# Performance work log

Measured on AMD Instinct MI355X. Metric: run time of the kernel, lower is better.

The kernel has to match this reference:

```python
import jax, jax.numpy as jnp
import numpy as np

S = 128    # spatial grid size
B = 2      # batch size
N = 60000  # number of points
EPS = 1e-4 # SparseConvNet BatchNorm eps
NEG = -3.0e38


def _conv3d(x, w, stride, padding):
    return jax.lax.conv_general_dilated(
        x, w, (stride,) * 3, padding,
        dimension_numbers=('NCDHW', 'OIDHW', 'NCDHW'))


def _pool2(x):
    # 2x2x2 max-pool, stride 2 (dims are powers of two)
    b, c, d, h, w = x.shape
    return x.reshape(b, c, d // 2, 2, h // 2, 2, w // 2, 2).max(axis=(3, 5, 7))


def _bn_relu(x, mask, gamma, beta):
    # BatchNormLeakyReLU(leakiness=0) over ACTIVE sites only (SCN semantics)
    n = mask.sum()
    mu = (x * mask).sum(axis=(0, 2, 3, 4)) / n
    mu_ = mu[None, :, None, None, None]
    var = (((x - mu_) ** 2) * mask).sum(axis=(0, 2, 3, 4)) / n
    scale = (gamma / jnp.sqrt(var + EPS))[None, :, None, None, None]
    y = (x - mu_) * scale + beta[None, :, None, None, None]
    return jnp.maximum(y, 0.0) * mask


def setup_inputs() -> dict:
    key = jax.random.key(0)
    ks = jax.random.split(key, 10)
    bi = jax.random.randint(ks[0], (N,), 0, B)
    xyz = jax.random.randint(ks[1], (N, 3), 0, S)
    feat = jax.random.normal(ks[2], (N, 1), dtype=jnp.float32)
    point_cloud = jnp.concatenate(
        [bi[:, None].astype(jnp.float32), xyz.astype(jnp.float32), feat], axis=1)

    def cw(k, o, i, ksz):
        return jax.random.normal(k, (o, i, ksz, ksz, ksz), dtype=jnp.float32) * np.float32(np.sqrt(2.0 / (i * ksz ** 3)))

    w_sub = cw(ks[3], 8, 1, 3)            # SubmanifoldConvolution(1->8, k=3)
    w0 = cw(ks[4], 16, 8, 2)              # Convolution(8->16, k=2, s=2)
    w1 = cw(ks[5], 32, 16, 2)
    w2 = cw(ks[6], 64, 32, 2)
    w3 = cw(ks[7], 128, 64, 2)
    g0, b0 = jnp.ones(8), jnp.zeros(8)
    g1, b1 = jnp.ones(16), jnp.zeros(16)
    g2, b2 = jnp.ones(32), jnp.zeros(32)
    g3, b3 = jnp.ones(64), jnp.zeros(64)
    Wc = jax.random.normal(ks[8], (2, 1024), dtype=jnp.float32) * np.float32(np.sqrt(1.0 / 1024))
    bc = jnp.zeros(2, dtype=jnp.float32)
    return dict(point_cloud=point_cloud, w_sub=w_sub, w0=w0, w1=w1, w2=w2, w3=w3,
                g0=g0, g1=g1, g2=g2, g3=g3, b0=b0, b1=b1, b2=b2, b3=b3, Wc=Wc, bc=bc)


def reference(point_cloud, w_sub, w0, w1, w2, w3,
              g0, g1, g2, g3, b0, b1, b2, b3, Wc, bc):
    bi = point_cloud[:, 0].astype(jnp.int32)
    ix = point_cloud[:, 1].astype(jnp.int32)
    iy = point_cloud[:, 2].astype(jnp.int32)
    iz = point_cloud[:, 3].astype(jnp.int32)
    f = point_cloud[:, 4]

    # InputLayer mode=3: scatter-sum duplicate coordinates into a dense grid
    grid = jnp.zeros((B, 1, S, S, S), jnp.float32).at[bi, 0, ix, iy, iz].add(f)
    mask = jnp.zeros((B, 1, S, S, S), jnp.float32).at[bi, 0, ix, iy, iz].set(1.0)

    # Submanifold conv k=3: dense conv (inactive feats are 0), output only at active sites
    h = _conv3d(grid, w_sub, 1, 'SAME') * mask

    for w, g, b in ((w0, g0, b0), (w1, g1, b1), (w2, g2, b2), (w3, g3, b3)):
        h = _bn_relu(h, mask, g, b)
        h = _conv3d(h, w, 2, 'VALID')
        mask = _pool2(mask)          # output site active iff any input in window active
        h = h * mask

    for _ in range(2):
        h = jnp.where(mask > 0, h, NEG)
        h = _pool2(h)
        mask = _pool2(mask)
        h = jnp.where(mask > 0, h, 0.0)

    # SparseToDense + flatten: [B,128,2,2,2] -> [B,1024]
    x = h.reshape(B, 128 * 8)
    rec_pos = jnp.maximum(x, 0.0) @ Wc.T + bc
    coords = point_cloud[:, 0:4]
    return coords, rec_pos
```

## Files before the change

### kernel.cpp

```cpp
#include <hip/hip_runtime.h>
#include <math.h>


#define NPTS 60000
#define NB 2
#define NEGF -3.0e38f
#define EPSF 1.0e-4f
#define MARKV 0xFFFEu
#define EMPTYV 0xFFFFu

constexpr int NV0 = NB * 128 * 128 * 128;
constexpr int NV1 = NB * 64 * 64 * 64;
constexpr int NV2 = NB * 32 * 32 * 32;
constexpr int NV3 = NB * 16 * 16 * 16;
constexpr int NV4 = NB * 8 * 8 * 8;

constexpr size_t OFF_CNT   = 0;
constexpr size_t OFF_BNSUM = 64;
constexpr size_t OFF_BNSS  = 1088;
constexpr size_t OFF_MASK5 = 2112;
constexpr size_t OFF_FGRID = 4096;
constexpr size_t OFF_IDX0  = OFF_FGRID + (size_t)NV0 * 4;
constexpr size_t OFF_IDX1  = OFF_IDX0 + (size_t)NV0 * 2;
constexpr size_t OFF_IDX2  = OFF_IDX1 + (size_t)NV1 * 2;
constexpr size_t OFF_IDX3  = OFF_IDX2 + (size_t)NV2 * 2;
constexpr size_t OFF_IDX4  = OFF_IDX3 + (size_t)NV3 * 2;
constexpr size_t OFF_LIST0 = OFF_IDX4 + (size_t)NV4 * 2;
constexpr size_t OFF_LIST1 = OFF_LIST0 + (size_t)NPTS * 4;
constexpr size_t OFF_LIST2 = OFF_LIST1 + (size_t)NPTS * 4;
constexpr size_t OFF_LIST3 = OFF_LIST2 + (size_t)NPTS * 4;
constexpr size_t OFF_LIST4 = OFF_LIST3 + (size_t)NV3 * 4;
constexpr size_t OFF_H0 = OFF_LIST4 + (size_t)NV4 * 4;
constexpr size_t OFF_H1 = OFF_H0 + (size_t)NPTS * 8 * 4;
constexpr size_t OFF_H2 = OFF_H1 + (size_t)NPTS * 16 * 4;
constexpr size_t OFF_H3 = OFF_H2 + (size_t)NPTS * 32 * 4;
constexpr size_t OFF_H4 = OFF_H3 + (size_t)NV3 * 64 * 4;
constexpr size_t OFF_H5 = OFF_H4 + (size_t)NV4 * 128 * 4;
constexpr size_t WS_END = OFF_H5 + (size_t)NB * 128 * 64 * 4;


__global__ __launch_bounds__(256) void k_scatter(const float* __restrict__ pc,
                                                 float* __restrict__ fgrid,
                                                 unsigned short* __restrict__ idx0,
                                                 unsigned short* __restrict__ idx1,
                                                 int* __restrict__ wsw,
                                                 float* __restrict__ out) {
  int gid = blockIdx.x * 256 + threadIdx.x;
  if (gid < 528) wsw[gid] = 0;
  idx1[gid] = (unsigned short)EMPTYV;
  if (gid < NPTS) {
    const float* p = pc + (size_t)gid * 5;
    float fb = p[0], fx = p[1], fy = p[2], fz = p[3], f = p[4];
    ((float4*)out)[gid] = make_float4(fb, fx, fy, fz);
    int b = (int)fb, x = (int)fx, y = (int)fy, z = (int)fz;
    int v = ((b * 128 + x) * 128 + y) * 128 + z;
    atomicAdd(&fgrid[v], f);
    idx0[v] = (unsigned short)MARKV;
  }
}

template <int SL, int NCLR16, int NCLRF>
__global__ __launch_bounds__(256) void k_cscan(unsigned short* __restrict__ idx,
                                               int* __restrict__ list,
                                               int* __restrict__ cnt, int slot,
                                               unsigned short* __restrict__ idx_par,
                                               unsigned short* __restrict__ clr16,
                                               float* __restrict__ clrf) {
  constexpr int NV = NB * SL * SL * SL;
  constexpr int NT = NV / 4;
  int gid = blockIdx.x * 256 + threadIdx.x;
  if (NCLR16 > 0 && gid < NCLR16) clr16[gid] = (unsigned short)EMPTYV;
  if (NCLRF > 0) {
    float4 z4 = make_float4(0.f, 0.f, 0.f, 0.f);
    for (int i = gid; i < NCLRF / 4; i += NT) ((float4*)clrf)[i] = z4;
  }
  ushort4 u = ((const ushort4*)idx)[gid];
  int p0 = (u.x == MARKV), p1 = (u.y == MARKV), p2 = (u.z == MARKV), p3 = (u.w == MARKV);
  int c = p0 + p1 + p2 + p3;
  int lane = threadIdx.x & 63, wid = threadIdx.x >> 6;
  int x = c;
#pragma unroll
  for (int off = 1; off < 64; off <<= 1) {
    int y = __shfl_up(x, off, 64);
    if (lane >= off) x += y;
  }
  __shared__ int sw[4];
  __shared__ int sbase;
  if (lane == 63) sw[wid] = x;
  __syncthreads();
  if (threadIdx.x == 0) {
    int r = 0;
#pragma unroll
    for (int w = 0; w < 4; w++) { int t = sw[w]; sw[w] = r; r += t; }
    sbase = r ? atomicAdd(&cnt[slot], r) : 0;
  }
  __syncthreads();
  if (!c) return;
  int my = sbase + sw[wid] + (x - c);
  int v0 = gid * 4;
  int pr[4] = {p0, p1, p2, p3};
#pragma unroll
  for (int j = 0; j < 4; j++) {
    if (pr[j]) {
      int v = v0 + j;
      idx[v] = (unsigned short)my;
      list[my] = v;
      my++;
      int z = v & (SL - 1), y = (v / SL) & (SL - 1),
          xx = (v / (SL * SL)) & (SL - 1), b = v / (SL * SL * SL);
      constexpr int SP = SL / 2;
      int pv = ((b * SP + (xx >> 1)) * SP + (y >> 1)) * SP + (z >> 1);
      idx_par[pv] = (unsigned short)MARKV;
    }
  }
}

__global__ __launch_bounds__(256) void k_ctail(unsigned short* __restrict__ idx3,
                                               unsigned short* __restrict__ idx4,
                                               int* __restrict__ list3,
                                               int* __restrict__ list4,
                                               int* __restrict__ cnt) {
  __shared__ int lc3, lc4;
  int tid = threadIdx.x, lane = tid & 63;
  if (tid == 0) { lc3 = 0; lc4 = 0; }
  __syncthreads();
  for (int v = tid; v < NV3; v += 256) {
    bool p = (idx3[v] == MARKV);
    unsigned long long m = __ballot(p);
    int wb = 0;
    if (lane == 0 && m) wb = atomicAdd(&lc3, __popcll(m));
    wb = __shfl(wb, 0, 64);
    if (p) {
      int id = wb + __popcll(m & ((1ull << lane) - 1));
      idx3[v] = (unsigned short)id;
      list3[id] = v;
      int z = v & 15, y = (v >> 4) & 15, x = (v >> 8) & 15, b = v >> 12;
      int pv = ((b * 8 + (x >> 1)) * 8 + (y >> 1)) * 8 + (z >> 1);
      idx4[pv] = (unsigned short)MARKV;
    }
  }
  __syncthreads();
  for (int v = tid; v < NV4; v += 256) {
    bool p = (idx4[v] == MARKV);
    unsigned long long m = __ballot(p);
    int wb = 0;
    if (lane == 0 && m) wb = atomicAdd(&lc4, __popcll(m));
    wb = __shfl(wb, 0, 64);
    if (p) {
      int id = wb + __popcll(m & ((1ull << lane) - 1));
      idx4[v] = (unsigned short)id;
      list4[id] = v;
    }
  }
  __syncthreads();
  if (tid == 0) { cnt[3] = lc3; cnt[4] = lc4; }
}

__global__ __launch_bounds__(256) void k_subconv(const float* __restrict__ fgrid,
                                                 const int* __restrict__ list0,
                                                 const int* __restrict__ cnt,
                                                 const float* __restrict__ wsub,
                                                 float* __restrict__ h0,
                                                 float* __restrict__ bnsum,
                                                 float* __restrict__ bnss) {
  int n = cnt[0];
  if ((int)(blockIdx.x * 256) >= n) return;
  __shared__ float wl[216];
  __shared__ float sbn[16];
  int tid = threadIdx.x;
  for (int i = tid; i < 216; i += 256) wl[i] = wsub[i];
  if (tid < 16) sbn[tid] = 0.f;
  __syncthreads();
  int id = blockIdx.x * 256 + tid;
  bool act = id < n;
  float acc[8] = {0, 0, 0, 0, 0, 0, 0, 0};
  if (act) {
    int v = list0[id];
    int z = v & 127, y = (v >> 7) & 127, x = (v >> 14) & 127, b = v >> 21;
    for (int kd = 0; kd < 3; kd++) {
      int xx = x + kd - 1;
      if ((unsigned)xx >= 128u) continue;
      for (int kh = 0; kh < 3; kh++) {
        int yy = y + kh - 1;
        if ((unsigned)yy >= 128u) continue;
        for (int kw = 0; kw < 3; kw++) {
          int zz = z + kw - 1;
          if ((unsigned)zz >= 128u) continue;
          float val = fgrid[((b * 128 + xx) * 128 + yy) * 128 + zz];
          if (val != 0.f) {
            int t = (kd * 3 + kh) * 3 + kw;
#pragma unroll
            for (int o = 0; o < 8; o++) acc[o] = fmaf(val, wl[o * 27 + t], acc[o]);
          }
        }
      }
    }
#pragma unroll
    for (int o = 0; o < 8; o++) h0[(size_t)id * 8 + o] = acc[o];
  }
  int lane = tid & 63;
#pragma unroll
  for (int o = 0; o < 8; o++) {
    float a = acc[o], q = a * a;
#pragma unroll
    for (int off = 32; off > 0; off >>= 1) {
      a += __shfl_down(a, off, 64);
      q += __shfl_down(q, off, 64);
    }
    if (lane == 0) { atomicAdd(&sbn[o], a); atomicAdd(&sbn[8 + o], q); }
  }
  __syncthreads();
  if (tid < 8) { atomicAdd(&bnsum[tid], sbn[tid]); atomicAdd(&bnss[tid], sbn[8 + tid]); }
}

template <int Ci, int Co, int OCCHUNK, int SLpar, int DENSE_OUT>
__global__ __launch_bounds__(256) void k_conv(const float* __restrict__ hin,
                                              const unsigned short* __restrict__ idxc,
                                              const int* __restrict__ listpar,
                                              const int* __restrict__ cnt,
                                              int slot_bn, int slot_par,
                                              const float* __restrict__ w,
                                              const float* __restrict__ bnsum_in,
                                              const float* __restrict__ bnss_in,
                                              const float* __restrict__ g,
                                              const float* __restrict__ beta,
                                              float* __restrict__ bnsum_out,
                                              float* __restrict__ bnss_out,
                                              float* __restrict__ hout) {
  constexpr int TPP = OCCHUNK / 8;
  constexpr int PPB = 256 / TPP;
  int n = cnt[slot_par];
  if ((int)(blockIdx.x * PPB) >= n) return;
  __shared__ float wl[Ci * 8 * OCCHUNK];
  __shared__ float sl[Ci], bl[Ci];
  __shared__ float bnl[2 * OCCHUNK];
  int tid = threadIdx.x;
  int ocbase = blockIdx.y * OCCHUNK;
  for (int i = tid; i < Ci * 8 * OCCHUNK; i += 256) {
    int ol = i % OCCHUNK;
    int it = i / OCCHUNK;
    int ci = it >> 3, t = it & 7;
    wl[i] = w[((size_t)(ocbase + ol) * Ci + ci) * 8 + t];
  }
  if (tid < Ci) {
    float nn = (float)cnt[slot_bn];
    float mu = bnsum_in[tid] / nn;
    float var = bnss_in[tid] / nn - mu * mu;
    var = fmaxf(var, 0.f);
    float sc = g[tid] / sqrtf(var + EPSF);
    sl[tid] = sc;
    bl[tid] = beta[tid] - mu * sc;
  }
  if (!DENSE_OUT && tid < 2 * OCCHUNK) bnl[tid] = 0.f;
  __syncthreads();
  int pid = blockIdx.x * PPB + tid / TPP;
  int og = tid % TPP;
  bool act = pid < n;
  float acc[8] = {0, 0, 0, 0, 0, 0, 0, 0};
  int Xc = 0, Yc = 0, Zc = 0, bb = 0;
  if (act) {
    int pv = listpar[pid];
    constexpr int SL = SLpar, SC = SLpar * 2;
    Zc = pv & (SL - 1);
    Yc = (pv / SL) & (SL - 1);
    Xc = (pv / (SL * SL)) & (SL - 1);
    bb = pv / (SL * SL * SL);
    for (int t = 0; t < 8; t++) {
      int kd = t >> 2, kh = (t >> 1) & 1, kw = t & 1;
      int cv = ((bb * SC + 2 * Xc + kd) * SC + 2 * Yc + kh) * SC + 2 * Zc + kw;
      unsigned e = idxc[cv];
      if (e >= 0xFFFEu) continue;
      const float* hp = hin + (size_t)e * Ci;
#pragma unroll
      for (int i = 0; i < Ci; i += 4) {
        float4 xv = *(const float4*)(hp + i);
        float y0 = fmaxf(fmaf(xv.x, sl[i + 0], bl[i + 0]), 0.f);
        float y1 = fmaxf(fmaf(xv.y, sl[i + 1], bl[i + 1]), 0.f);
        float y2 = fmaxf(fmaf(xv.z, sl[i + 2], bl[i + 2]), 0.f);
        float y3 = fmaxf(fmaf(xv.w, sl[i + 3], bl[i + 3]), 0.f);
        const float* wp0 = &wl[((i + 0) * 8 + t) * OCCHUNK + og * 8];
        const float* wp1 = &wl[((i + 1) * 8 + t) * OCCHUNK + og * 8];
        const float* wp2 = &wl[((i + 2) * 8 + t) * OCCHUNK + og * 8];
        const float* wp3 = &wl[((i + 3) * 8 + t) * OCCHUNK + og * 8];
#pragma unroll
        for (int o = 0; o < 8; o++) {
          acc[o] = fmaf(y0, wp0[o], acc[o]);
          acc[o] = fmaf(y1, wp1[o], acc[o]);
          acc[o] = fmaf(y2, wp2[o], acc[o]);
          acc[o] = fmaf(y3, wp3[o], acc[o]);
        }
      }
    }
    if (!DENSE_OUT) {
      float* op = hout + (size_t)pid * Co + ocbase + og * 8;
#pragma unroll
      for (int o = 0; o < 8; o++) op[o] = acc[o];
    } else {
      int sp = (Xc * 8 + Yc) * 8 + Zc;
#pragma unroll
      for (int o = 0; o < 8; o++)
        hout[((size_t)bb * 128 + ocbase + og * 8 + o) * 512 + sp] = acc[o];
    }
  }
  if (!DENSE_OUT) {
    int lane = tid & 63;
#pragma unroll
    for (int o = 0; o < 8; o++) {
      float a = acc[o], q = a * a;
#pragma unroll
      for (int off = TPP; off < 64; off <<= 1) {
        a += __shfl_down(a, off, 64);
        q += __shfl_down(q, off, 64);
      }
      if (lane < TPP) {
        atomicAdd(&bnl[lane * 8 + o], a);
        atomicAdd(&bnl[OCCHUNK + lane * 8 + o], q);
      }
    }
    __syncthreads();
    if (tid < OCCHUNK) {
      atomicAdd(&bnsum_out[ocbase + tid], bnl[tid]);
      atomicAdd(&bnss_out[ocbase + tid], bnl[OCCHUNK + tid]);
    }
  }
}

__global__ __launch_bounds__(256) void k_pool1(const float* __restrict__ h4,
                                               const unsigned short* __restrict__ idx4,
                                               float* __restrict__ h5,
                                               int* __restrict__ mask5) {
  int tid = blockIdx.x * 256 + threadIdx.x;
  int sp = tid & 63;
  int c = (tid >> 6) & 127;
  int b = tid >> 13;
  int Z = sp & 3, Y = (sp >> 2) & 3, X = sp >> 4;
  float m = NEGF;
  int any = 0;
#pragma unroll
  for (int t = 0; t < 8; t++) {
    int kd = t >> 2, kh = (t >> 1) & 1, kw = t & 1;
    int csp = ((2 * X + kd) * 8 + 2 * Y + kh) * 8 + 2 * Z + kw;
    if (idx4[b * 512 + csp] != EMPTYV) {
      any = 1;
      m = fmaxf(m, h4[((size_t)b * 128 + c) * 512 + csp]);
    }
  }
  h5[((size_t)b * 128 + c) * 64 + sp] = any ? m : 0.f;
  if (c == 0) mask5[b * 64 + sp] = any;
}

__global__ __launch_bounds__(256) void k_tail(const float* __restrict__ h5,
                                              const int* __restrict__ mask5,
                                              const float* __restrict__ Wc,
                                              const float* __restrict__ bcv,
                                              float* __restrict__ out) {
  __shared__ float h6s[2048];
  int tid = threadIdx.x;
#pragma unroll
  for (int j = 0; j < 8; j++) {
    int e = tid * 8 + j;
    int sp = e & 7, c = (e >> 3) & 127, b = e >> 10;
    int Z = sp & 1, Y = (sp >> 1) & 1, X = sp >> 2;
    float m = NEGF;
    int any = 0;
#pragma unroll
    for (int t = 0; t < 8; t++) {
      int kd = t >> 2, kh = (t >> 1) & 1, kw = t & 1;
      int csp = ((2 * X + kd) * 4 + 2 * Y + kh) * 4 + 2 * Z + kw;
      if (mask5[b * 64 + csp]) {
        any = 1;
        m = fmaxf(m, h5[((size_t)b * 128 + c) * 64 + csp]);
      }
    }
    h6s[e] = any ? fmaxf(m, 0.f) : 0.f;
  }
  __syncthreads();
  int wave = tid >> 6, lane = tid & 63;
  int b = wave >> 1, o = wave & 1;
  float s = 0.f;
  for (int k = lane; k < 1024; k += 64) s += h6s[b * 1024 + k] * Wc[o * 1024 + k];
#pragma unroll
  for (int off = 32; off > 0; off >>= 1) s += __shfl_down(s, off, 64);
  if (lane == 0) out[240000 + b * 2 + o] = s + bcv[o];
}


extern "C" void kernel_launch(void* const* d_in, const int* in_sizes, int n_in,
                              void* d_out, int out_size, void* d_ws, size_t ws_size,
                              hipStream_t stream) {
  const float* pc   = (const float*)d_in[0];
  const float* wsub = (const float*)d_in[1];
  const float* w0   = (const float*)d_in[2];
  const float* w1   = (const float*)d_in[3];
  const float* w2   = (const float*)d_in[4];
  const float* w3   = (const float*)d_in[5];
  const float* g0   = (const float*)d_in[6];
  const float* g1   = (const float*)d_in[7];
  const float* g2   = (const float*)d_in[8];
  const float* g3   = (const float*)d_in[9];
  const float* b0   = (const float*)d_in[10];
  const float* b1   = (const float*)d_in[11];
  const float* b2   = (const float*)d_in[12];
  const float* b3   = (const float*)d_in[13];
  const float* Wc   = (const float*)d_in[14];
  const float* bc   = (const float*)d_in[15];
  float* out = (float*)d_out;

  char* base = (char*)d_ws;
  int*   cnt   = (int*)(base + OFF_CNT);
  float* bnsum = (float*)(base + OFF_BNSUM);
  float* bnss  = (float*)(base + OFF_BNSS);
  int*   mask5 = (int*)(base + OFF_MASK5);
  float* fgrid = (float*)(base + OFF_FGRID);
  unsigned short* idx0 = (unsigned short*)(base + OFF_IDX0);
  unsigned short* idx1 = (unsigned short*)(base + OFF_IDX1);
  unsigned short* idx2 = (unsigned short*)(base + OFF_IDX2);
  unsigned short* idx3 = (unsigned short*)(base + OFF_IDX3);
  unsigned short* idx4 = (unsigned short*)(base + OFF_IDX4);
  int* list0 = (int*)(base + OFF_LIST0);
  int* list1 = (int*)(base + OFF_LIST1);
  int* list2 = (int*)(base + OFF_LIST2);
  int* list3 = (int*)(base + OFF_LIST3);
  int* list4 = (int*)(base + OFF_LIST4);
  float* h0 = (float*)(base + OFF_H0);
  float* h1 = (float*)(base + OFF_H1);
  float* h2 = (float*)(base + OFF_H2);
  float* h3 = (float*)(base + OFF_H3);
  float* h4 = (float*)(base + OFF_H4);
  float* h5 = (float*)(base + OFF_H5);

  hipMemsetAsync(fgrid, 0, (size_t)NV0 * 4, stream);
  hipMemsetAsync(idx0, 0xFF, (size_t)NV0 * 2, stream);

  k_scatter<<<NV1 / 256, 256, 0, stream>>>(pc, fgrid, idx0, idx1, (int*)base, out);

  k_cscan<128, NV2, 0><<<NV0 / 4 / 256, 256, 0, stream>>>(
      idx0, list0, cnt, 0, idx1, idx2, (float*)nullptr);
  k_cscan<64, NV3 + NV4, 0><<<NV1 / 4 / 256, 256, 0, stream>>>(
      idx1, list1, cnt, 1, idx2, idx3, (float*)nullptr);
  k_cscan<32, 0, NV4 * 128><<<NV2 / 4 / 256, 256, 0, stream>>>(
      idx2, list2, cnt, 2, idx3, (unsigned short*)nullptr, h4);
  k_ctail<<<1, 256, 0, stream>>>(idx3, idx4, list3, list4, cnt);

  k_subconv<<<(NPTS + 255) / 256, 256, 0, stream>>>(fgrid, list0, cnt, wsub, h0,
                                                    bnsum + 0, bnss + 0);

  k_conv<8, 16, 16, 64, 0><<<dim3((NPTS + 127) / 128, 1), 256, 0, stream>>>(
      h0, idx0, list1, cnt, 0, 1, w0, bnsum + 0, bnss + 0, g0, b0,
      bnsum + 64, bnss + 64, h1);
  k_conv<16, 32, 32, 32, 0><<<dim3((NPTS + 63) / 64, 1), 256, 0, stream>>>(
      h1, idx1, list2, cnt, 1, 2, w1, bnsum + 64, bnss + 64, g1, b1,
      bnsum + 128, bnss + 128, h2);
  k_conv<32, 64, 32, 16, 0><<<dim3((NV3 + 63) / 64, 2), 256, 0, stream>>>(
      h2, idx2, list3, cnt, 2, 3, w2, bnsum + 128, bnss + 128, g2, b2,
      bnsum + 192, bnss + 192, h3);
  k_conv<64, 128, 16, 8, 1><<<dim3((NV4 + 127) / 128, 8), 256, 0, stream>>>(
      h3, idx3, list4, cnt, 3, 4, w3, bnsum + 192, bnss + 192, g3, b3,
      (float*)nullptr, (float*)nullptr, h4);

  k_pool1<<<(NB * 128 * 64) / 256, 256, 0, stream>>>(h4, idx4, h5, mask5);
  k_tail<<<1, 256, 0, stream>>>(h5, mask5, Wc, bc, out);
}
```

Before: 317.6 us.

## Shard BN atomics across slots, persistent scan blocks, split subconv taps

Batch-norm statistics are now accumulated into 16 slot-strided copies chosen by block index, and the consumer sums the slots. This cuts same-address atomic contention. The compaction scans now run with far fewer blocks, each thread handling several ushort4 chunks, which reduces the number of global counter atomics. The submanifold conv splits the 27 taps across 4 threads per point and combines the partial sums with xor shuffles. Clears are vectorized, and the workspace layout is enlarged to hold the slots. The costs are more scan work per thread and an extra reduction pass in each conv prologue.

```diff
diff --git a/kernel.cpp b/kernel.cpp
--- a/kernel.cpp
+++ b/kernel.cpp
@@ -8,6 +8,7 @@
 #define EPSF 1.0e-4f
 #define MARKV 0xFFFEu
 #define EMPTYV 0xFFFFu
+#define NSLOT 16
 
 constexpr int NV0 = NB * 128 * 128 * 128;
 constexpr int NV1 = NB * 64 * 64 * 64;
@@ -16,10 +17,10 @@
 constexpr int NV4 = NB * 8 * 8 * 8;
 
 constexpr size_t OFF_CNT   = 0;
-constexpr size_t OFF_BNSUM = 64;
-constexpr size_t OFF_BNSS  = 1088;
-constexpr size_t OFF_MASK5 = 2112;
-constexpr size_t OFF_FGRID = 4096;
+constexpr size_t OFF_BNSUM = 1024;
+constexpr size_t OFF_BNSS  = 17408;
+constexpr size_t OFF_MASK5 = 33792;
+constexpr size_t OFF_FGRID = 65536;
 constexpr size_t OFF_IDX0  = OFF_FGRID + (size_t)NV0 * 4;
 constexpr size_t OFF_IDX1  = OFF_IDX0 + (size_t)NV0 * 2;
 constexpr size_t OFF_IDX2  = OFF_IDX1 + (size_t)NV1 * 2;
@@ -46,8 +47,14 @@
                                                  int* __restrict__ wsw,
                                                  float* __restrict__ out) {
   int gid = blockIdx.x * 256 + threadIdx.x;
-  if (gid < 528) wsw[gid] = 0;
-  idx1[gid] = (unsigned short)EMPTYV;
+  if (gid < 2112) {
+    ((int4*)wsw)[gid] = make_int4(0, 0, 0, 0);
+  }
+  if (gid < NV1 / 4) {
+    ((ushort4*)idx1)[gid] =
+        make_ushort4((unsigned short)EMPTYV, (unsigned short)EMPTYV,
+                     (unsigned short)EMPTYV, (unsigned short)EMPTYV);
+  }
   if (gid < NPTS) {
     const float* p = pc + (size_t)gid * 5;
     float fb = p[0], fx = p[1], fy = p[2], fz = p[3], f = p[4];
@@ -59,7 +66,7 @@
   }
 }
 
-template <int SL, int NCLR16, int NCLRF>
+template <int SL, int NBLK, int NCLR16, int NCLRF>
 __global__ __launch_bounds__(256) void k_cscan(unsigned short* __restrict__ idx,
                                                int* __restrict__ list,
                                                int* __restrict__ cnt, int slot,
@@ -67,17 +74,29 @@
                                                unsigned short* __restrict__ clr16,
                                                float* __restrict__ clrf) {
   constexpr int NV = NB * SL * SL * SL;
-  constexpr int NT = NV / 4;
-  int gid = blockIdx.x * 256 + threadIdx.x;
-  if (NCLR16 > 0 && gid < NCLR16) clr16[gid] = (unsigned short)EMPTYV;
+  constexpr int NT = NBLK * 256;
+  constexpr int IT = NV / 4 / NT;
+  int tid = threadIdx.x;
+  int gid = blockIdx.x * 256 + tid;
+  if (NCLR16 > 0) {
+    ushort4 e4 = make_ushort4((unsigned short)EMPTYV, (unsigned short)EMPTYV,
+                              (unsigned short)EMPTYV, (unsigned short)EMPTYV);
+    for (int i = gid; i < NCLR16 / 4; i += NT) ((ushort4*)clr16)[i] = e4;
+  }
   if (NCLRF > 0) {
     float4 z4 = make_float4(0.f, 0.f, 0.f, 0.f);
     for (int i = gid; i < NCLRF / 4; i += NT) ((float4*)clrf)[i] = z4;
   }
-  ushort4 u = ((const ushort4*)idx)[gid];
-  int p0 = (u.x == MARKV), p1 = (u.y == MARKV), p2 = (u.z == MARKV), p3 = (u.w == MARKV);
-  int c = p0 + p1 + p2 + p3;
-  int lane = threadIdx.x & 63, wid = threadIdx.x >> 6;
+  const ushort4* idx4p = (const ushort4*)idx;
+  ushort4 uu[IT];
+  int c = 0;
+#pragma unroll
+  for (int it = 0; it < IT; it++) {
+    uu[it] = idx4p[gid + it * NT];
+    c += (uu[it].x == MARKV) + (uu[it].y == MARKV) + (uu[it].z == MARKV) +
+         (uu[it].w == MARKV);
+  }
+  int lane = tid & 63, wid = tid >> 6;
   int x = c;
 #pragma unroll
   for (int off = 1; off < 64; off <<= 1) {
@@ -88,7 +107,7 @@
   __shared__ int sbase;
   if (lane == 63) sw[wid] = x;
   __syncthreads();
-  if (threadIdx.x == 0) {
+  if (tid == 0) {
     int r = 0;
 #pragma unroll
     for (int w = 0; w < 4; w++) { int t = sw[w]; sw[w] = r; r += t; }
@@ -97,20 +116,23 @@
   __syncthreads();
   if (!c) return;
   int my = sbase + sw[wid] + (x - c);
-  int v0 = gid * 4;
-  int pr[4] = {p0, p1, p2, p3};
-#pragma unroll
-  for (int j = 0; j < 4; j++) {
-    if (pr[j]) {
-      int v = v0 + j;
-      idx[v] = (unsigned short)my;
-      list[my] = v;
-      my++;
-      int z = v & (SL - 1), y = (v / SL) & (SL - 1),
-          xx = (v / (SL * SL)) & (SL - 1), b = v / (SL * SL * SL);
-      constexpr int SP = SL / 2;
-      int pv = ((b * SP + (xx >> 1)) * SP + (y >> 1)) * SP + (z >> 1);
-      idx_par[pv] = (unsigned short)MARKV;
+#pragma unroll
+  for (int it = 0; it < IT; it++) {
+    unsigned short us[4] = {uu[it].x, uu[it].y, uu[it].z, uu[it].w};
+    int v0 = (gid + it * NT) * 4;
+#pragma unroll
+    for (int j = 0; j < 4; j++) {
+      if (us[j] == MARKV) {
+        int v = v0 + j;
+        idx[v] = (unsigned short)my;
+        list[my] = v;
+        my++;
+        int z = v & (SL - 1), y = (v / SL) & (SL - 1),
+            xx = (v / (SL * SL)) & (SL - 1), b = v / (SL * SL * SL);
+        constexpr int SP = SL / 2;
+        int pv = ((b * SP + (xx >> 1)) * SP + (y >> 1)) * SP + (z >> 1);
+        idx_par[pv] = (unsigned short)MARKV;
+      }
     }
   }
 }
@@ -164,44 +186,46 @@
                                                  float* __restrict__ bnsum,
                                                  float* __restrict__ bnss) {
   int n = cnt[0];
-  if ((int)(blockIdx.x * 256) >= n) return;
+  if ((int)(blockIdx.x * 64) >= n) return;
   __shared__ float wl[216];
   __shared__ float sbn[16];
   int tid = threadIdx.x;
   for (int i = tid; i < 216; i += 256) wl[i] = wsub[i];
   if (tid < 16) sbn[tid] = 0.f;
   __syncthreads();
-  int id = blockIdx.x * 256 + tid;
-  bool act = id < n;
+  int pid = blockIdx.x * 64 + (tid >> 2);
+  int sub = tid & 3;
+  bool act = pid < n;
   float acc[8] = {0, 0, 0, 0, 0, 0, 0, 0};
   if (act) {
-    int v = list0[id];
+    int v = list0[pid];
     int z = v & 127, y = (v >> 7) & 127, x = (v >> 14) & 127, b = v >> 21;
-    for (int kd = 0; kd < 3; kd++) {
-      int xx = x + kd - 1;
-      if ((unsigned)xx >= 128u) continue;
-      for (int kh = 0; kh < 3; kh++) {
-        int yy = y + kh - 1;
-        if ((unsigned)yy >= 128u) continue;
-        for (int kw = 0; kw < 3; kw++) {
-          int zz = z + kw - 1;
-          if ((unsigned)zz >= 128u) continue;
-          float val = fgrid[((b * 128 + xx) * 128 + yy) * 128 + zz];
-          if (val != 0.f) {
-            int t = (kd * 3 + kh) * 3 + kw;
-#pragma unroll
-            for (int o = 0; o < 8; o++) acc[o] = fmaf(val, wl[o * 27 + t], acc[o]);
-          }
+    int t0 = sub * 7, t1 = t0 + 7 > 27 ? 27 : t0 + 7;
+    for (int t = t0; t < t1; t++) {
+      int kd = t / 9, kh = (t / 3) % 3, kw = t % 3;
+      int xx = x + kd - 1, yy = y + kh - 1, zz = z + kw - 1;
+      if ((unsigned)xx < 128u && (unsigned)yy < 128u && (unsigned)zz < 128u) {
+        float val = fgrid[((b * 128 + xx) * 128 + yy) * 128 + zz];
+        if (val != 0.f) {
+#pragma unroll
+          for (int o = 0; o < 8; o++) acc[o] = fmaf(val, wl[o * 27 + t], acc[o]);
         }
       }
     }
-#pragma unroll
-    for (int o = 0; o < 8; o++) h0[(size_t)id * 8 + o] = acc[o];
+  }
+#pragma unroll
+  for (int o = 0; o < 8; o++) {
+    acc[o] += __shfl_xor(acc[o], 1, 64);
+    acc[o] += __shfl_xor(acc[o], 2, 64);
+  }
+  if (act) {
+    ((float2*)(h0 + (size_t)pid * 8))[sub] = make_float2(acc[sub * 2], acc[sub * 2 + 1]);
   }
   int lane = tid & 63;
 #pragma unroll
   for (int o = 0; o < 8; o++) {
-    float a = acc[o], q = a * a;
+    float a = ((o >> 1) == sub && act) ? acc[o] : 0.f;
+    float q = a * a;
 #pragma unroll
     for (int off = 32; off > 0; off >>= 1) {
       a += __shfl_down(a, off, 64);
@@ -210,7 +234,11 @@
     if (lane == 0) { atomicAdd(&sbn[o], a); atomicAdd(&sbn[8 + o], q); }
   }
   __syncthreads();
-  if (tid < 8) { atomicAdd(&bnsum[tid], sbn[tid]); atomicAdd(&bnss[tid], sbn[8 + tid]); }
+  if (tid < 8) {
+    int s = (blockIdx.x & (NSLOT - 1)) * 64;
+    atomicAdd(&bnsum[s + tid], sbn[tid]);
+    atomicAdd(&bnss[s + tid], sbn[8 + tid]);
+  }
 }
 
 template <int Ci, int Co, int OCCHUNK, int SLpar, int DENSE_OUT>
@@ -244,9 +272,11 @@
   }
   if (tid < Ci) {
     float nn = (float)cnt[slot_bn];
-    float mu = bnsum_in[tid] / nn;
-    float var = bnss_in[tid] / nn - mu * mu;
-    var = fmaxf(var, 0.f);
+    float s = 0.f, ss = 0.f;
+#pragma unroll
+    for (int k = 0; k < NSLOT; k++) { s += bnsum_in[k * 64 + tid]; ss += bnss_in[k * 64 + tid]; }
+    float mu = s / nn;
+    float var = fmaxf(ss / nn - mu * mu, 0.f);
     float sc = g[tid] / sqrtf(var + EPSF);
     sl[tid] = sc;
     bl[tid] = beta[tid] - mu * sc;
@@ -319,8 +349,9 @@
     }
     __syncthreads();
     if (tid < OCCHUNK) {
-      atomicAdd(&bnsum_out[ocbase + tid], bnl[tid]);
-      atomicAdd(&bnss_out[ocbase + tid], bnl[OCCHUNK + tid]);
+      int s = (blockIdx.x & (NSLOT - 1)) * 64;
+      atomicAdd(&bnsum_out[s + ocbase + tid], bnl[tid]);
+      atomicAdd(&bnss_out[s + ocbase + tid], bnl[OCCHUNK + tid]);
     }
   }
 }
@@ -434,28 +465,28 @@
 
   k_scatter<<<NV1 / 256, 256, 0, stream>>>(pc, fgrid, idx0, idx1, (int*)base, out);
 
-  k_cscan<128, NV2, 0><<<NV0 / 4 / 256, 256, 0, stream>>>(
+  k_cscan<128, 128, NV2, 0><<<128, 256, 0, stream>>>(
       idx0, list0, cnt, 0, idx1, idx2, (float*)nullptr);
-  k_cscan<64, NV3 + NV4, 0><<<NV1 / 4 / 256, 256, 0, stream>>>(
+  k_cscan<64, 64, NV3 + NV4, 0><<<64, 256, 0, stream>>>(
       idx1, list1, cnt, 1, idx2, idx3, (float*)nullptr);
-  k_cscan<32, 0, NV4 * 128><<<NV2 / 4 / 256, 256, 0, stream>>>(
+  k_cscan<32, 16, 0, NV4 * 128><<<16, 256, 0, stream>>>(
       idx2, list2, cnt, 2, idx3, (unsigned short*)nullptr, h4);
   k_ctail<<<1, 256, 0, stream>>>(idx3, idx4, list3, list4, cnt);
 
-  k_subconv<<<(NPTS + 255) / 256, 256, 0, stream>>>(fgrid, list0, cnt, wsub, h0,
-                                                    bnsum + 0, bnss + 0);
+  k_subconv<<<(NPTS * 4 + 255) / 256, 256, 0, stream>>>(fgrid, list0, cnt, wsub,
+                                                        h0, bnsum, bnss);
 
   k_conv<8, 16, 16, 64, 0><<<dim3((NPTS + 127) / 128, 1), 256, 0, stream>>>(
-      h0, idx0, list1, cnt, 0, 1, w0, bnsum + 0, bnss + 0, g0, b0,
-      bnsum + 64, bnss + 64, h1);
+      h0, idx0, list1, cnt, 0, 1, w0, bnsum, bnss, g0, b0,
+      bnsum + 1024, bnss + 1024, h1);
   k_conv<16, 32, 32, 32, 0><<<dim3((NPTS + 63) / 64, 1), 256, 0, stream>>>(
-      h1, idx1, list2, cnt, 1, 2, w1, bnsum + 64, bnss + 64, g1, b1,
-      bnsum + 128, bnss + 128, h2);
+      h1, idx1, list2, cnt, 1, 2, w1, bnsum + 1024, bnss + 1024, g1, b1,
+      bnsum + 2048, bnss + 2048, h2);
   k_conv<32, 64, 32, 16, 0><<<dim3((NV3 + 63) / 64, 2), 256, 0, stream>>>(
-      h2, idx2, list3, cnt, 2, 3, w2, bnsum + 128, bnss + 128, g2, b2,
-      bnsum + 192, bnss + 192, h3);
+      h2, idx2, list3, cnt, 2, 3, w2, bnsum + 2048, bnss + 2048, g2, b2,
+      bnsum + 3072, bnss + 3072, h3);
   k_conv<64, 128, 16, 8, 1><<<dim3((NV4 + 127) / 128, 8), 256, 0, stream>>>(
-      h3, idx3, list4, cnt, 3, 4, w3, bnsum + 192, bnss + 192, g3, b3,
+      h3, idx3, list4, cnt, 3, 4, w3, bnsum + 3072, bnss + 3072, g3, b3,
       (float*)nullptr, (float*)nullptr, h4);
 
   k_pool1<<<(NB * 128 * 64) / 256, 256, 0, stream>>>(h4, idx4, h5, mask5);
```

After: 273.6 us. 13.8% less time.
